# Kernel optimization log

Hardware: AMD Instinct MI355X
Metric: run time of the kernel (lower is better)

Reference implementation:

```python
import jax, jax.numpy as jnp
import numpy as np

C = 1.0
TAU = 1.0
LE = 1.0
LH = 1.0
LN_EPS = 1e-5

def _safe_norm(x, keepdims=False):
    return jnp.clip(jnp.sqrt(jnp.sum(x * x, axis=-1, keepdims=keepdims)), 1e-15)

def _project_to_ball(x, c, eps=1e-5):
    sqrt_c = c ** 0.5
    norm = _safe_norm(x, keepdims=True)
    max_norm = (1.0 - eps) / sqrt_c
    scale = jnp.where(norm > max_norm, max_norm / norm, 1.0)
    return x * scale

def _lambda_x(x, c):
    x = _project_to_ball(x, c)
    x2 = jnp.sum(x * x, axis=-1, keepdims=True)
    return 2.0 / jnp.clip(1.0 - c * x2, 1e-15)

def _mobius_add(x, y, c):
    x = _project_to_ball(x, c)
    y = _project_to_ball(y, c)
    x2 = jnp.sum(x * x, axis=-1, keepdims=True)
    y2 = jnp.sum(y * y, axis=-1, keepdims=True)
    xy = jnp.sum(x * y, axis=-1, keepdims=True)
    num = (1 + 2 * c * xy + c * y2) * x + (1 - c * x2) * y
    den = 1 + 2 * c * xy + c ** 2 * x2 * y2
    return num / jnp.clip(den, 1e-15)

def _exp_map_x(x, v, c):
    sqrt_c = c ** 0.5
    lam = _lambda_x(x, c)
    vnorm = _safe_norm(v, keepdims=True)
    v_dir = v / vnorm
    factor = jnp.tanh(lam * sqrt_c * vnorm / 2.0) / sqrt_c
    out = _mobius_add(x, v_dir * factor, c)
    return _project_to_ball(out, c)

def _log_map_x(x, y, c):
    sqrt_c = c ** 0.5
    lam = _lambda_x(x, c)
    u = _mobius_add(-x, y, c)
    unorm = _safe_norm(u, keepdims=True)
    u_dir = u / unorm
    arg = jnp.minimum(sqrt_c * unorm, 1 - 1e-7)
    scale = 2.0 / (lam * sqrt_c) * jnp.arctanh(arg)
    return scale * u_dir

def _poincare_distance_sq(x, y, c):
    sqrt_c = c ** 0.5
    x = _project_to_ball(x, c)
    y = _project_to_ball(y, c)
    diff = _mobius_add(-x, y, c)
    norm = _safe_norm(diff, keepdims=False)
    arg = jnp.minimum(sqrt_c * norm, 1 - 1e-7)
    dist = 2.0 / sqrt_c * jnp.arctanh(arg)
    return dist * dist

def setup_inputs() -> dict:
    key = jax.random.key(0)
    ks = jax.random.split(key, 6)
    B, N, L, A, de, dh, z_dim = 8, 8, 64, 64, 128, 64, 128
    z_e, z_h = z_dim // 2 + z_dim % 2, z_dim // 2
    return {
        "curr_rho_batch": jax.random.normal(ks[0], (B, A, de), jnp.float32),
        "curr_hyp_emb": 0.1 * jax.random.normal(ks[1], (B, dh), jnp.float32),
        "demo_rho_batch": jax.random.normal(ks[2], (B, N, L, A, de), jnp.float32),
        "demo_hyp_emb": 0.1 * jax.random.normal(ks[3], (B, N, L, dh), jnp.float32),
        "We": 0.02 * jax.random.normal(ks[4], (z_e, de), jnp.float32),
        "Wh": 0.02 * jax.random.normal(ks[5], (z_h, dh), jnp.float32),
        "ln_gamma": jnp.ones((z_dim,), jnp.float32),
        "ln_beta": jnp.zeros((z_dim,), jnp.float32),
    }

def reference(curr_rho_batch, curr_hyp_emb, demo_rho_batch, demo_hyp_emb, We, Wh, ln_gamma, ln_beta):
    B, A, de = curr_rho_batch.shape
    _, N, L, _, _ = demo_rho_batch.shape
    M = N * L
    dh = curr_hyp_emb.shape[-1]
    demo_rho_flat = demo_rho_batch.reshape(B, M, A, de)   # [B,M,A,de]
    demo_hyp_flat = demo_hyp_emb.reshape(B, M, dh)        # [B,M,dh]
    # Euclidean squared distances: [B,M,A] -> [B,A,M]
    e_diff_sq = jnp.sum((curr_rho_batch[:, None, :, :] - demo_rho_flat) ** 2, axis=-1)
    e_diff_sq = jnp.transpose(e_diff_sq, (0, 2, 1))
    # Hyperbolic squared distances: [B,M]
    dH2 = _poincare_distance_sq(curr_hyp_emb[:, None, :], demo_hyp_flat, C)
    scores = -(LH * dH2[:, None, :] + LE * e_diff_sq) / max(TAU, 1e-8)  # [B,A,M]
    alpha = jax.nn.softmax(scores, axis=-1)
    # Euclidean aggregation
    e_out = jnp.einsum('bam,bmad->bad', alpha, demo_rho_flat)  # [B,A,de]
    # Hyperbolic Karcher-mean step
    log_vecs = _log_map_x(curr_hyp_emb[:, None, :], demo_hyp_flat, C)  # [B,M,dh]
    v = jnp.einsum('bam,bmd->bad', alpha, log_vecs)  # [B,A,dh]
    x_ba = jnp.broadcast_to(curr_hyp_emb[:, None, :], (B, A, dh))
    h_out = _exp_map_x(x_ba, v, C)  # [B,A,dh]
    z = jnp.concatenate([e_out @ We.T, h_out @ Wh.T], axis=-1)  # [B,A,z_dim]
    mean = jnp.mean(z, axis=-1, keepdims=True)
    var = jnp.var(z, axis=-1, keepdims=True)
    z = (z - mean) / jnp.sqrt(var + LN_EPS) * ln_gamma + ln_beta
    return z
```

## Files before the change

### kernel.cpp

```cpp
#include <hip/hip_runtime.h>

#define DEV __device__ __forceinline__

constexpr int A_ = 64, DE = 128, M_ = 512, DH = 64;

DEV float wred_sum64(float v) {
#pragma unroll
    for (int o = 1; o < 64; o <<= 1) v += __shfl_xor(v, o, 64);
    return v;
}

__global__ __launch_bounds__(256) void k_hyp(const float* __restrict__ curr_hyp,
                                             const float* __restrict__ demo_hyp,
                                             float* __restrict__ dH2,
                                             float* __restrict__ logv) {
    const int lane = threadIdx.x & 63;
    const int r    = (blockIdx.x << 2) + (threadIdx.x >> 6);
    const int b    = r >> 9;

    float x = curr_hyp[(b << 6) + lane];
    float y = demo_hyp[((size_t)r << 6) + lane];
    const float mx = 1.0f - 1e-5f;

    float x2r = wred_sum64(x * x);
    float xn  = fmaxf(sqrtf(x2r), 1e-15f);
    float sx  = xn > mx ? mx / xn : 1.0f;
    x *= sx;
    float x2 = x2r * sx * sx;
    float y2r = wred_sum64(y * y);
    float yn  = fmaxf(sqrtf(y2r), 1e-15f);
    float sy  = yn > mx ? mx / yn : 1.0f;
    y *= sy;
    float y2 = y2r * sy * sy;

    float xy = wred_sum64(x * y);
    float num = (1.f - 2.f * xy + y2) * (-x) + (1.f - x2) * y;
    float den = fmaxf(1.f - 2.f * xy + x2 * y2, 1e-15f);
    float u   = num / den;

    float u2  = wred_sum64(u * u);
    float un  = fmaxf(sqrtf(u2), 1e-15f);
    float arg = fminf(un, 1.f - 1e-7f);
    float at  = 0.5f * __logf((1.f + arg) / (1.f - arg));

    if (lane == 0) dH2[r] = 4.f * at * at;

    float lamden = fmaxf(1.f - x2, 1e-15f);
    float ls     = lamden * at / un;
    logv[((size_t)r << 6) + lane] = ls * u;
}

__global__ __launch_bounds__(512, 4) void k_main(const float* __restrict__ curr_rho,
                                                 const float* __restrict__ demo_rho,
                                                 const float* __restrict__ curr_hyp,
                                                 const float* __restrict__ dH2,
                                                 const float* __restrict__ logv,
                                                 const float* __restrict__ We,
                                                 const float* __restrict__ Wh,
                                                 const float* __restrict__ gamma,
                                                 const float* __restrict__ beta,
                                                 float* __restrict__ out) {
    __shared__ float lds_sc[512];
    __shared__ float lds_dh[512];
    __shared__ float redmax[8];
    __shared__ float redsum[8];
    __shared__ __align__(16) float accbuf[8 * 132];
    __shared__ float vpart[8][64];
    __shared__ float eh[192];

    const int t    = threadIdx.x;
    const int lane = t & 63;
    const int wv   = t >> 6;
    const int dp   = lane & 15;
    const int mq   = lane >> 4;
    const int blk  = blockIdx.x;
    const int b    = blk >> 6, a = blk & 63;

    lds_dh[t] = dH2[(b << 9) + t];

    float qf[8];
    {
        float4 q0 = *(const float4*)(curr_rho + (size_t)blk * DE + dp * 8);
        float4 q1 = *(const float4*)(curr_rho + (size_t)blk * DE + dp * 8 + 4);
        qf[0] = q0.x; qf[1] = q0.y; qf[2] = q0.z; qf[3] = q0.w;
        qf[4] = q1.x; qf[5] = q1.y; qf[6] = q1.z; qf[7] = q1.w;
    }

    const size_t rowStride = (size_t)A_ * DE;
    const float* p = demo_rho + (((size_t)b * M_ + wv * 64 + mq) * A_ + a) * DE + dp * 8;

    float mx = -1e30f, sm = 0.f, ac[8];
#pragma unroll
    for (int j = 0; j < 8; j++) ac[j] = 0.f;

    float4 c0 = *(const float4*)p;
    float4 c1 = *(const float4*)(p + 4);

    for (int i = 0; i < 16; ++i) {
        const float* pn = p + 4 * rowStride;
        float4 n0, n1;
        if (i < 15) { n0 = *(const float4*)pn; n1 = *(const float4*)(pn + 4); }

        float kf[8];
        kf[0] = c0.x; kf[1] = c0.y; kf[2] = c0.z; kf[3] = c0.w;
        kf[4] = c1.x; kf[5] = c1.y; kf[6] = c1.z; kf[7] = c1.w;

        float ps = 0.f;
#pragma unroll
        for (int j = 0; j < 8; j++) { float d = qf[j] - kf[j]; ps = fmaf(d, d, ps); }
        ps += __shfl_xor(ps, 1, 64);
        ps += __shfl_xor(ps, 2, 64);
        ps += __shfl_xor(ps, 4, 64);
        ps += __shfl_xor(ps, 8, 64);

        const int ml = wv * 64 + mq + 4 * i;
        float sc = -(lds_dh[ml] + ps);
        if (dp == 0) lds_sc[ml] = sc;

        float nm = fmaxf(mx, sc);
        float r  = __expf(mx - nm);
        float w  = __expf(sc - nm);
        sm = sm * r + w;
#pragma unroll
        for (int j = 0; j < 8; j++) ac[j] = fmaf(ac[j], r, w * kf[j]);
        mx = nm;

        p = pn; c0 = n0; c1 = n1;
    }

#pragma unroll
    for (int off = 16; off < 64; off <<= 1) {
        float mxo = __shfl_xor(mx, off, 64);
        float smo = __shfl_xor(sm, off, 64);
        float aco[8];
#pragma unroll
        for (int j = 0; j < 8; j++) aco[j] = __shfl_xor(ac[j], off, 64);
        float nm = fmaxf(mx, mxo);
        float r1 = __expf(mx - nm), r2 = __expf(mxo - nm);
        sm = sm * r1 + smo * r2;
#pragma unroll
        for (int j = 0; j < 8; j++) ac[j] = ac[j] * r1 + aco[j] * r2;
        mx = nm;
    }
    if (lane == 0) { redmax[wv] = mx; redsum[wv] = sm; }
    __syncthreads();

    float gmax = redmax[0];
#pragma unroll
    for (int w = 1; w < 8; w++) gmax = fmaxf(gmax, redmax[w]);
    float gsum = 0.f;
#pragma unroll
    for (int w = 0; w < 8; w++) gsum += redsum[w] * __expf(redmax[w] - gmax);
    const float inv = 1.f / gsum;

    float resc = __expf(mx - gmax);
    if (lane < 16) {
        *(float4*)&accbuf[wv * 132 + dp * 8] =
            make_float4(ac[0] * resc, ac[1] * resc, ac[2] * resc, ac[3] * resc);
        *(float4*)&accbuf[wv * 132 + dp * 8 + 4] =
            make_float4(ac[4] * resc, ac[5] * resc, ac[6] * resc, ac[7] * resc);
    }

    {
        const float* lvb = logv + ((size_t)(b * M_) + wv * 64) * DH;
        float vacc = 0.f;
#pragma unroll 8
        for (int i = 0; i < 64; ++i) {
            float al = __expf(lds_sc[wv * 64 + i] - gmax);
            vacc = fmaf(al, lvb[(size_t)i * DH + lane], vacc);
        }
        vpart[wv][lane] = vacc * inv;
    }
    __syncthreads();

    if (t < 128) {
        float s = 0.f;
#pragma unroll
        for (int g = 0; g < 8; g++) s += accbuf[g * 132 + t];
        eh[t] = s * inv;
    }
    __syncthreads();

    if (wv == 0) {
        float v = 0.f;
#pragma unroll
        for (int w = 0; w < 8; w++) v += vpart[w][lane];

        const float mxb = 1.0f - 1e-5f;
        float x = curr_hyp[(b << 6) + lane];
        float x2r = wred_sum64(x * x);
        float xn  = fmaxf(sqrtf(x2r), 1e-15f);
        float sx  = xn > mxb ? mxb / xn : 1.f;
        x *= sx;
        float x2 = x2r * sx * sx;
        float lamden = fmaxf(1.f - x2, 1e-15f);

        float v2 = wred_sum64(v * v);
        float vn = fmaxf(sqrtf(v2), 1e-15f);
        float targ   = vn / lamden;
        float e2     = __expf(2.f * targ);
        float factor = 1.f - 2.f / (e2 + 1.f);
        float wvv    = v * (factor / vn);

        float w2 = wred_sum64(wvv * wvv);
        float xw = wred_sum64(x * wvv);
        float num = (1.f + 2.f * xw + w2) * x + (1.f - x2) * wvv;
        float den = fmaxf(1.f + 2.f * xw + x2 * w2, 1e-15f);
        float h   = num / den;
        float h2  = wred_sum64(h * h);
        float hn  = fmaxf(sqrtf(h2), 1e-15f);
        float shh = hn > mxb ? mxb / hn : 1.f;
        h *= shh;
        eh[128 + lane] = h;

        float ze = 0.f;
        const float* werow = We + lane * 128;
#pragma unroll
        for (int d0 = 0; d0 < 128; d0 += 4) {
            float4 wv4 = *(const float4*)(werow + d0);
            ze = fmaf(eh[d0 + 0], wv4.x, ze);
            ze = fmaf(eh[d0 + 1], wv4.y, ze);
            ze = fmaf(eh[d0 + 2], wv4.z, ze);
            ze = fmaf(eh[d0 + 3], wv4.w, ze);
        }
        float zh = 0.f;
        const float* whrow = Wh + lane * 64;
#pragma unroll
        for (int d0 = 0; d0 < 64; d0 += 4) {
            float4 wv4 = *(const float4*)(whrow + d0);
            zh = fmaf(eh[128 + d0 + 0], wv4.x, zh);
            zh = fmaf(eh[128 + d0 + 1], wv4.y, zh);
            zh = fmaf(eh[128 + d0 + 2], wv4.z, zh);
            zh = fmaf(eh[128 + d0 + 3], wv4.w, zh);
        }
        float ssum = wred_sum64(ze + zh);
        float mean = ssum * (1.f / 128.f);
        float sq   = wred_sum64(ze * ze + zh * zh);
        float var  = sq * (1.f / 128.f) - mean * mean;
        float rinv = rsqrtf(var + 1e-5f);
        float oe = (ze - mean) * rinv * gamma[lane] + beta[lane];
        float oh = (zh - mean) * rinv * gamma[64 + lane] + beta[64 + lane];
        out[(size_t)blk * 128 + lane]      = oe;
        out[(size_t)blk * 128 + 64 + lane] = oh;
    }
}

extern "C" void kernel_launch(void* const* d_in, const int* in_sizes, int n_in,
                              void* d_out, int out_size, void* d_ws, size_t ws_size,
                              hipStream_t stream) {
    const float* curr_rho = (const float*)d_in[0];
    const float* curr_hyp = (const float*)d_in[1];
    const float* demo_rho = (const float*)d_in[2];
    const float* demo_hyp = (const float*)d_in[3];
    const float* We       = (const float*)d_in[4];
    const float* Wh       = (const float*)d_in[5];
    const float* gamma    = (const float*)d_in[6];
    const float* beta     = (const float*)d_in[7];
    float* out = (float*)d_out;

    float* ws   = (float*)d_ws;
    float* dH2  = ws;
    float* logv = ws + 4096;

    k_hyp<<<1024, 256, 0, stream>>>(curr_hyp, demo_hyp, dH2, logv);
    k_main<<<512, 512, 0, stream>>>(curr_rho, demo_rho, curr_hyp, dH2, logv,
                                    We, Wh, gamma, beta, out);
}
```

Baseline: 230.9 us.

## Split attention over M chunks with contiguous demo_rho reads and separate merge kernel

Replaces the per-(b,a) kernel, which read demo_rho rows scattered across M, with a kernel that gives each block a chunk of 8 demo rows for all 64 anchors. Each block reads contiguous memory and keeps an online-softmax partial per anchor, covering both the Euclidean and the log-vector sums, which is written to a workspace. A new merge kernel combines the 64 partials per (b,a) and runs the exp-map, projection and LayerNorm epilogue. The aim is coalesced streaming of the dominant 128 MB demo_rho read. The cost is an extra launch and roughly 25 MB of partial-result traffic.

New measurement: 276.4 us. +19.7%, slower.

```diff
diff --git a/kernel.cpp b/kernel.cpp
--- a/kernel.cpp
+++ b/kernel.cpp
@@ -3,10 +3,16 @@
 #define DEV __device__ __forceinline__
 
 constexpr int A_ = 64, DE = 128, M_ = 512, DH = 64;
+constexpr int REC = 196;
 
 DEV float wred_sum64(float v) {
 #pragma unroll
     for (int o = 1; o < 64; o <<= 1) v += __shfl_xor(v, o, 64);
+    return v;
+}
+DEV float wred_max64(float v) {
+#pragma unroll
+    for (int o = 1; o < 64; o <<= 1) v = fmaxf(v, __shfl_xor(v, o, 64));
     return v;
 }
 
@@ -50,142 +56,141 @@
     logv[((size_t)r << 6) + lane] = ls * u;
 }
 
-__global__ __launch_bounds__(512, 4) void k_main(const float* __restrict__ curr_rho,
+__global__ __launch_bounds__(512, 4) void k_part(const float* __restrict__ curr_rho,
                                                  const float* __restrict__ demo_rho,
-                                                 const float* __restrict__ curr_hyp,
                                                  const float* __restrict__ dH2,
                                                  const float* __restrict__ logv,
-                                                 const float* __restrict__ We,
-                                                 const float* __restrict__ Wh,
-                                                 const float* __restrict__ gamma,
-                                                 const float* __restrict__ beta,
-                                                 float* __restrict__ out) {
-    __shared__ float lds_sc[512];
-    __shared__ float lds_dh[512];
-    __shared__ float redmax[8];
-    __shared__ float redsum[8];
-    __shared__ __align__(16) float accbuf[8 * 132];
-    __shared__ float vpart[8][64];
+                                                 float* __restrict__ part) {
+    __shared__ __align__(16) float q_lds[64 * 128];
+    __shared__ __align__(16) float lv_lds[8 * 64];
+    __shared__ float dh_lds[8];
+
+    const int t   = threadIdx.x;
+    const int blk = blockIdx.x;
+    const int b   = blk >> 6, mc = blk & 63;
+    const int lane = t & 63, w = t >> 6;
+    const int h = lane >> 5, hl = lane & 31;
+
+    {
+        const float* qsrc = curr_rho + (size_t)b * A_ * DE;
+#pragma unroll
+        for (int i = 0; i < 4; i++)
+            *(float4*)&q_lds[i * 2048 + t * 4] = *(const float4*)(qsrc + i * 2048 + t * 4);
+        if (t < 128)
+            *(float4*)&lv_lds[t * 4] =
+                *(const float4*)(logv + ((size_t)b * M_ + mc * 8) * DH + t * 4);
+        if (t < 8) dh_lds[t] = dH2[b * M_ + mc * 8 + t];
+    }
+    __syncthreads();
+
+    float qf[4][4];
+#pragma unroll
+    for (int s = 0; s < 4; s++) {
+        int a = 8 * w + 2 * s + h;
+        float4 q = *(const float4*)&q_lds[a * 128 + hl * 4];
+        qf[s][0] = q.x; qf[s][1] = q.y; qf[s][2] = q.z; qf[s][3] = q.w;
+    }
+
+    float mAcc[4], sAcc[4], eAcc[4][4], vAcc[4][2];
+#pragma unroll
+    for (int s = 0; s < 4; s++) {
+        mAcc[s] = -1e30f; sAcc[s] = 0.f;
+        eAcc[s][0] = eAcc[s][1] = eAcc[s][2] = eAcc[s][3] = 0.f;
+        vAcc[s][0] = vAcc[s][1] = 0.f;
+    }
+
+    const float* base = demo_rho + (((size_t)b * M_ + mc * 8) * A_ + 8 * w) * DE;
+
+    float4 cur[4];
+#pragma unroll
+    for (int s = 0; s < 4; s++) cur[s] = *(const float4*)(base + s * 256 + lane * 4);
+
+    for (int m = 0; m < 8; ++m) {
+        float4 nxt[4];
+        if (m < 7) {
+            const float* nb = base + (size_t)(m + 1) * 8192;
+#pragma unroll
+            for (int s = 0; s < 4; s++) nxt[s] = *(const float4*)(nb + s * 256 + lane * 4);
+        }
+        float2 lvv = *(const float2*)&lv_lds[m * 64 + hl * 2];
+        float dh = dh_lds[m];
+#pragma unroll
+        for (int s = 0; s < 4; s++) {
+            float kf[4] = {cur[s].x, cur[s].y, cur[s].z, cur[s].w};
+            float ps = 0.f;
+#pragma unroll
+            for (int j = 0; j < 4; j++) { float d = qf[s][j] - kf[j]; ps = fmaf(d, d, ps); }
+            ps += __shfl_xor(ps, 1, 64);
+            ps += __shfl_xor(ps, 2, 64);
+            ps += __shfl_xor(ps, 4, 64);
+            ps += __shfl_xor(ps, 8, 64);
+            ps += __shfl_xor(ps, 16, 64);
+            float sc = -(dh + ps);
+
+            float nm = fmaxf(mAcc[s], sc);
+            float r  = __expf(mAcc[s] - nm);
+            float wt = __expf(sc - nm);
+            sAcc[s] = sAcc[s] * r + wt;
+#pragma unroll
+            for (int j = 0; j < 4; j++) eAcc[s][j] = fmaf(eAcc[s][j], r, wt * kf[j]);
+            vAcc[s][0] = fmaf(vAcc[s][0], r, wt * lvv.x);
+            vAcc[s][1] = fmaf(vAcc[s][1], r, wt * lvv.y);
+            mAcc[s] = nm;
+        }
+#pragma unroll
+        for (int s = 0; s < 4; s++) cur[s] = nxt[s];
+    }
+
+#pragma unroll
+    for (int s = 0; s < 4; s++) {
+        int a = 8 * w + 2 * s + h;
+        float* rec = part + ((size_t)(b * 64 + a) * 64 + mc) * REC;
+        *(float4*)(rec + hl * 4) = make_float4(eAcc[s][0], eAcc[s][1], eAcc[s][2], eAcc[s][3]);
+        *(float2*)(rec + 128 + hl * 2) = make_float2(vAcc[s][0], vAcc[s][1]);
+        if (hl == 0) { rec[192] = mAcc[s]; rec[193] = sAcc[s]; }
+    }
+}
+
+__global__ __launch_bounds__(256) void k_merge(const float* __restrict__ part,
+                                               const float* __restrict__ curr_hyp,
+                                               const float* __restrict__ We,
+                                               const float* __restrict__ Wh,
+                                               const float* __restrict__ gamma,
+                                               const float* __restrict__ beta,
+                                               float* __restrict__ out) {
+    __shared__ float f_lds[64];
+    __shared__ float gsum_s;
     __shared__ float eh[192];
-
-    const int t    = threadIdx.x;
-    const int lane = t & 63;
-    const int wv   = t >> 6;
-    const int dp   = lane & 15;
-    const int mq   = lane >> 4;
-    const int blk  = blockIdx.x;
-    const int b    = blk >> 6, a = blk & 63;
-
-    lds_dh[t] = dH2[(b << 9) + t];
-
-    float qf[8];
-    {
-        float4 q0 = *(const float4*)(curr_rho + (size_t)blk * DE + dp * 8);
-        float4 q1 = *(const float4*)(curr_rho + (size_t)blk * DE + dp * 8 + 4);
-        qf[0] = q0.x; qf[1] = q0.y; qf[2] = q0.z; qf[3] = q0.w;
-        qf[4] = q1.x; qf[5] = q1.y; qf[6] = q1.z; qf[7] = q1.w;
-    }
-
-    const size_t rowStride = (size_t)A_ * DE;
-    const float* p = demo_rho + (((size_t)b * M_ + wv * 64 + mq) * A_ + a) * DE + dp * 8;
-
-    float mx = -1e30f, sm = 0.f, ac[8];
-#pragma unroll
-    for (int j = 0; j < 8; j++) ac[j] = 0.f;
-
-    float4 c0 = *(const float4*)p;
-    float4 c1 = *(const float4*)(p + 4);
-
-    for (int i = 0; i < 16; ++i) {
-        const float* pn = p + 4 * rowStride;
-        float4 n0, n1;
-        if (i < 15) { n0 = *(const float4*)pn; n1 = *(const float4*)(pn + 4); }
-
-        float kf[8];
-        kf[0] = c0.x; kf[1] = c0.y; kf[2] = c0.z; kf[3] = c0.w;
-        kf[4] = c1.x; kf[5] = c1.y; kf[6] = c1.z; kf[7] = c1.w;
-
-        float ps = 0.f;
-#pragma unroll
-        for (int j = 0; j < 8; j++) { float d = qf[j] - kf[j]; ps = fmaf(d, d, ps); }
-        ps += __shfl_xor(ps, 1, 64);
-        ps += __shfl_xor(ps, 2, 64);
-        ps += __shfl_xor(ps, 4, 64);
-        ps += __shfl_xor(ps, 8, 64);
-
-        const int ml = wv * 64 + mq + 4 * i;
-        float sc = -(lds_dh[ml] + ps);
-        if (dp == 0) lds_sc[ml] = sc;
-
-        float nm = fmaxf(mx, sc);
-        float r  = __expf(mx - nm);
-        float w  = __expf(sc - nm);
-        sm = sm * r + w;
-#pragma unroll
-        for (int j = 0; j < 8; j++) ac[j] = fmaf(ac[j], r, w * kf[j]);
-        mx = nm;
-
-        p = pn; c0 = n0; c1 = n1;
-    }
-
-#pragma unroll
-    for (int off = 16; off < 64; off <<= 1) {
-        float mxo = __shfl_xor(mx, off, 64);
-        float smo = __shfl_xor(sm, off, 64);
-        float aco[8];
-#pragma unroll
-        for (int j = 0; j < 8; j++) aco[j] = __shfl_xor(ac[j], off, 64);
-        float nm = fmaxf(mx, mxo);
-        float r1 = __expf(mx - nm), r2 = __expf(mxo - nm);
-        sm = sm * r1 + smo * r2;
-#pragma unroll
-        for (int j = 0; j < 8; j++) ac[j] = ac[j] * r1 + aco[j] * r2;
-        mx = nm;
-    }
-    if (lane == 0) { redmax[wv] = mx; redsum[wv] = sm; }
+    __shared__ float vv[64];
+
+    const int t = threadIdx.x, w = t >> 6, lane = t & 63;
+    const int blk = blockIdx.x, b = blk >> 6;
+    const float* pbase = part + (size_t)blk * 64 * REC;
+
+    if (w == 0) {
+        float mx = pbase[lane * REC + 192];
+        float sm = pbase[lane * REC + 193];
+        float g  = wred_max64(mx);
+        float f  = __expf(mx - g);
+        float gs = wred_sum64(sm * f);
+        f_lds[lane] = f;
+        if (lane == 0) gsum_s = gs;
+    }
     __syncthreads();
-
-    float gmax = redmax[0];
-#pragma unroll
-    for (int w = 1; w < 8; w++) gmax = fmaxf(gmax, redmax[w]);
-    float gsum = 0.f;
-#pragma unroll
-    for (int w = 0; w < 8; w++) gsum += redsum[w] * __expf(redmax[w] - gmax);
-    const float inv = 1.f / gsum;
-
-    float resc = __expf(mx - gmax);
-    if (lane < 16) {
-        *(float4*)&accbuf[wv * 132 + dp * 8] =
-            make_float4(ac[0] * resc, ac[1] * resc, ac[2] * resc, ac[3] * resc);
-        *(float4*)&accbuf[wv * 132 + dp * 8 + 4] =
-            make_float4(ac[4] * resc, ac[5] * resc, ac[6] * resc, ac[7] * resc);
-    }
-
-    {
-        const float* lvb = logv + ((size_t)(b * M_) + wv * 64) * DH;
-        float vacc = 0.f;
-#pragma unroll 8
-        for (int i = 0; i < 64; ++i) {
-            float al = __expf(lds_sc[wv * 64 + i] - gmax);
-            vacc = fmaf(al, lvb[(size_t)i * DH + lane], vacc);
-        }
-        vpart[wv][lane] = vacc * inv;
+    const float inv = 1.f / gsum_s;
+
+    if (t < 192) {
+        float acc = 0.f;
+#pragma unroll 4
+        for (int mc = 0; mc < 64; ++mc) acc = fmaf(pbase[mc * REC + t], f_lds[mc], acc);
+        acc *= inv;
+        if (t < 128) eh[t] = acc;
+        else vv[t - 128] = acc;
     }
     __syncthreads();
 
-    if (t < 128) {
-        float s = 0.f;
-#pragma unroll
-        for (int g = 0; g < 8; g++) s += accbuf[g * 132 + t];
-        eh[t] = s * inv;
-    }
-    __syncthreads();
-
-    if (wv == 0) {
-        float v = 0.f;
-#pragma unroll
-        for (int w = 0; w < 8; w++) v += vpart[w][lane];
-
+    if (w == 0) {
+        float v = vv[lane];
         const float mxb = 1.0f - 1e-5f;
         float x = curr_hyp[(b << 6) + lane];
         float x2r = wred_sum64(x * x);
@@ -206,12 +211,12 @@
         float xw = wred_sum64(x * wvv);
         float num = (1.f + 2.f * xw + w2) * x + (1.f - x2) * wvv;
         float den = fmaxf(1.f + 2.f * xw + x2 * w2, 1e-15f);
-        float h   = num / den;
-        float h2  = wred_sum64(h * h);
+        float hq  = num / den;
+        float h2  = wred_sum64(hq * hq);
         float hn  = fmaxf(sqrtf(h2), 1e-15f);
         float shh = hn > mxb ? mxb / hn : 1.f;
-        h *= shh;
-        eh[128 + lane] = h;
+        hq *= shh;
+        eh[128 + lane] = hq;
 
         float ze = 0.f;
         const float* werow = We + lane * 128;
@@ -261,8 +266,9 @@
     float* ws   = (float*)d_ws;
     float* dH2  = ws;
     float* logv = ws + 4096;
+    float* part = ws + 4096 + 262144;
 
     k_hyp<<<1024, 256, 0, stream>>>(curr_hyp, demo_hyp, dH2, logv);
-    k_main<<<512, 512, 0, stream>>>(curr_rho, demo_rho, curr_hyp, dH2, logv,
-                                    We, Wh, gamma, beta, out);
-}
+    k_part<<<512, 512, 0, stream>>>(curr_rho, demo_rho, dH2, logv, part);
+    k_merge<<<512, 256, 0, stream>>>(part, curr_hyp, We, Wh, gamma, beta, out);
+}
```
